# Optimization experiments

Measured on AMD Instinct MI355X. Metric: run time of the kernel, lower is better.

## Reference

```python
import jax, jax.numpy as jnp
import numpy as np
import math

D = 768
H = 12
HD = D // H  # 64
B, N = 16, 1024
EPS = 1e-5


def _rope(x, cos, sin):
    # x: [B,N,H,hd]; cos,sin: [1,N,1,hd]
    x1, x2 = x[..., ::2], x[..., 1::2]
    return jnp.concatenate(
        [x1 * cos[..., ::2] - x2 * sin[..., ::2],
         x1 * sin[..., 1::2] + x2 * cos[..., 1::2]], axis=-1)


def setup_inputs() -> dict:
    key = jax.random.key(0)
    ks = jax.random.split(key, 8)
    s = 1.0 / math.sqrt(D)  # xavier-ish scale
    return {
        "x": jax.random.normal(ks[0], (B, N, D), jnp.float32),
        "rope_emb": jax.random.normal(ks[1], (N, HD), jnp.float32),
        "ln_w": jnp.ones((D,), jnp.float32),
        "ln_b": jnp.zeros((D,), jnp.float32),
        "enc_w": jax.random.normal(ks[2], (D, D), jnp.float32) * s,
        "enc_b": jnp.zeros((D,), jnp.float32),
        "qk_w": jax.random.normal(ks[3], (D, D), jnp.float32) * s,
        "qk_b": jnp.zeros((D,), jnp.float32),
        "v_w": jax.random.normal(ks[4], (D, D), jnp.float32) * s,
        "v_b": jnp.zeros((D,), jnp.float32),
        "out_w": jax.random.normal(ks[5], (D, D), jnp.float32) * s,
        "out_b": jnp.zeros((D,), jnp.float32),
        "gate_w": jax.random.normal(ks[6], (D, D), jnp.float32) * s,
        "gate_b": jnp.zeros((D,), jnp.float32),
    }


def reference(x, rope_emb, ln_w, ln_b, enc_w, enc_b, qk_w, qk_b,
              v_w, v_b, out_w, out_b, gate_w, gate_b):
    b, n, d = x.shape
    # Pre-LayerNorm
    mu = jnp.mean(x, axis=-1, keepdims=True)
    var = jnp.mean(jnp.square(x - mu), axis=-1, keepdims=True)
    x_norm = (x - mu) / jnp.sqrt(var + EPS) * ln_w + ln_b
    # sparse latent encoder
    x_latent = jax.nn.relu(x_norm @ enc_w.T + enc_b)
    qk = (x_latent @ qk_w.T + qk_b).reshape(b, n, H, HD)
    v = (x_latent @ v_w.T + v_b).reshape(b, n, H, HD)
    ang = rope_emb[:, :HD]
    cos = jnp.cos(ang)[None, :, None, :]
    sin = jnp.sin(ang)[None, :, None, :]
    qk = _rope(qk, cos, sin)
    # raw (softmax-free) attention, Q=K
    scores = jnp.einsum('bnhd,bmhd->bhnm', qk, qk) / math.sqrt(HD)
    attn = jnp.einsum('bhnm,bmhd->bnhd', scores, v).reshape(b, n, d)
    attn = attn @ out_w.T + out_b
    gate = jax.nn.sigmoid(x_norm @ gate_w.T + gate_b)
    return x + gate * attn
```

## Files before the change

### kernel.cpp

```cpp
#include <hip/hip_runtime.h>

typedef __bf16 bf16;
typedef __bf16 bf16x2 __attribute__((ext_vector_type(2)));
typedef __bf16 bf16x4 __attribute__((ext_vector_type(4)));
typedef __bf16 bf16x8 __attribute__((ext_vector_type(8)));
typedef float floatx4 __attribute__((ext_vector_type(4)));

#define DD 768
#define NH 12
#define HDIM 64
#define BB 16
#define NN 1024
#define MTOT (BB*NN)
#define WELEM (DD*DD)

#define ABUF 16384
#define BBUF 8192
#define TBUF (ABUF + BBUF)

__device__ __forceinline__ void async_cp16(const void* g, void* l) {
  __builtin_amdgcn_global_load_lds((const __attribute__((address_space(1))) void*)g,
                                   (__attribute__((address_space(3))) void*)l, 16, 0, 0);
}

__global__ __launch_bounds__(256) void prep_kernel(
    const float* __restrict__ x, const float* __restrict__ lnw,
    const float* __restrict__ lnb, bf16* __restrict__ A,
    const float* __restrict__ w0, const float* __restrict__ w1,
    const float* __restrict__ w2, const float* __restrict__ w3,
    const float* __restrict__ w4, bf16* __restrict__ Wb,
    const float* __restrict__ rope, float* __restrict__ tabs) {
  int blk = blockIdx.x;
  int tid = threadIdx.x;
  if (blk < 4096) {
    int row = blk * 4 + (tid >> 6);
    int lane = tid & 63;
    const float4* xr = (const float4*)(x + (size_t)row * DD);
    float4 v[3];
    float s = 0.f;
#pragma unroll
    for (int i = 0; i < 3; i++) {
      v[i] = xr[lane + 64 * i];
      s += v[i].x + v[i].y + v[i].z + v[i].w;
    }
#pragma unroll
    for (int o = 32; o; o >>= 1) s += __shfl_xor(s, o);
    float mu = s * (1.f / 768.f);
    float vs = 0.f;
#pragma unroll
    for (int i = 0; i < 3; i++) {
      float dx;
      dx = v[i].x - mu; vs += dx * dx;
      dx = v[i].y - mu; vs += dx * dx;
      dx = v[i].z - mu; vs += dx * dx;
      dx = v[i].w - mu; vs += dx * dx;
    }
#pragma unroll
    for (int o = 32; o; o >>= 1) vs += __shfl_xor(vs, o);
    float rstd = rsqrtf(vs * (1.f / 768.f) + 1e-5f);
    const float4* wv = (const float4*)lnw;
    const float4* bv = (const float4*)lnb;
    bf16* Ar = A + (size_t)row * DD;
#pragma unroll
    for (int i = 0; i < 3; i++) {
      int c4 = lane + 64 * i;
      float4 ww = wv[c4], bb = bv[c4];
      bf16x4 pk;
      pk[0] = (bf16)((v[i].x - mu) * rstd * ww.x + bb.x);
      pk[1] = (bf16)((v[i].y - mu) * rstd * ww.y + bb.y);
      pk[2] = (bf16)((v[i].z - mu) * rstd * ww.z + bb.z);
      pk[3] = (bf16)((v[i].w - mu) * rstd * ww.w + bb.w);
      *(bf16x4*)(Ar + c4 * 4) = pk;
    }
  } else if (blk < 4096 + 2880) {
    int i = (blk - 4096) * 256 + tid;
    int which = i / (WELEM / 4);
    int off = (i % (WELEM / 4)) * 4;
    const float* s = which == 0 ? w0 : which == 1 ? w1 : which == 2 ? w2 : which == 3 ? w3 : w4;
    float4 v = *(const float4*)(s + off);
    bf16x4 pk;
    pk[0] = (bf16)v.x; pk[1] = (bf16)v.y; pk[2] = (bf16)v.z; pk[3] = (bf16)v.w;
    *(bf16x4*)(Wb + (size_t)i * 4) = pk;
  } else {
    int i = (blk - 6976) * 256 + tid;
    int j = i >> 10, n = i & 1023;
    float a = rope[n * 64 + j];
    float s, c;
    __sincosf(a, &s, &c);
    tabs[i] = c;
    tabs[65536 + i] = s;
  }
}

template<int EPI>
__device__ __forceinline__ void gemm_body(
    int bm, int bn, int bnl,
    const bf16* __restrict__ Aop, const bf16* __restrict__ W,
    const float* __restrict__ bias,
    bf16* __restrict__ Cb, bf16* __restrict__ CT, float* __restrict__ Cf,
    const float* __restrict__ Xres, const bf16* __restrict__ Gate,
    const float* __restrict__ tabs, bf16* smem) {
  int tid = threadIdx.x;
  int w = tid >> 6, lane = tid & 63;
  int quad = lane >> 4, l16 = lane & 15;
  int wm = w >> 1, wn = w & 1;
  int sr = lane >> 3;
  int scg = (lane & 7) ^ sr;
  int swz = l16 & 7;

  const bf16* Ag = Aop + (size_t)(bm * 256) * DD;
  const bf16* Bg = W + (size_t)(bn * 128) * DD;
  const bf16* srcA = Ag + (size_t)(w * 8 + sr) * DD + scg * 8;
  const bf16* srcB = Bg + (size_t)(w * 8 + sr) * DD + scg * 8;

  floatx4 acc[4][4];
#pragma unroll
  for (int i = 0; i < 4; i++)
#pragma unroll
    for (int j = 0; j < 4; j++)
      acc[i][j] = (floatx4){0.f, 0.f, 0.f, 0.f};

  auto stageH0 = [&](int k0, bf16* buf) {
    async_cp16(srcA + (size_t)0 * (64 * DD) + k0, buf + (w + 0) * 512);
    async_cp16(srcA + (size_t)1 * (64 * DD) + k0, buf + (w + 8) * 512);
    async_cp16(srcB + k0, buf + ABUF + w * 512);
  };
  auto stageH1 = [&](int k0, bf16* buf) {
    async_cp16(srcA + (size_t)2 * (64 * DD) + k0, buf + (w + 16) * 512);
    async_cp16(srcA + (size_t)3 * (64 * DD) + k0, buf + (w + 24) * 512);
    async_cp16(srcB + (size_t)64 * DD + k0, buf + ABUF + (w + 8) * 512);
  };

  stageH0(0, smem);               stageH1(0, smem);
  stageH0(64, smem + TBUF);       stageH1(64, smem + TBUF);

#pragma unroll
  for (int t = 0; t < 12; t++) {
    if (t < 11) asm volatile("s_waitcnt vmcnt(6)" ::: "memory");
    else        asm volatile("s_waitcnt vmcnt(0)" ::: "memory");
    __builtin_amdgcn_s_barrier();
    __builtin_amdgcn_sched_barrier(0);

    const bf16* Ab = smem + (t % 3) * TBUF;
    const bf16* Bb = Ab + ABUF;
#pragma unroll
    for (int ks = 0; ks < 2; ks++) {
      int cg = (ks * 4 + quad) ^ swz;
      bf16x8 a[4], b[4];
#pragma unroll
      for (int i = 0; i < 4; i++) a[i] = *(const bf16x8*)&Ab[(wm * 64 + i * 16 + l16) * 64 + cg * 8];
#pragma unroll
      for (int i = 0; i < 4; i++) b[i] = *(const bf16x8*)&Bb[(wn * 64 + i * 16 + l16) * 64 + cg * 8];
      if (t < 10) {
        if (ks == 0) stageH0((t + 2) * 64, smem + ((t + 2) % 3) * TBUF);
        else         stageH1((t + 2) * 64, smem + ((t + 2) % 3) * TBUF);
      }
      __builtin_amdgcn_s_barrier();
      __builtin_amdgcn_sched_barrier(0);
      asm volatile("s_waitcnt lgkmcnt(0)" ::: "memory");
      __builtin_amdgcn_sched_barrier(0);
      __builtin_amdgcn_s_setprio(1);
      if (EPI == 2) {
#pragma unroll
        for (int mi = 0; mi < 4; mi++)
#pragma unroll
          for (int ni = 0; ni < 4; ni++)
            acc[mi][ni] = __builtin_amdgcn_mfma_f32_16x16x32_bf16(a[mi], b[ni], acc[mi][ni], 0, 0, 0);
      } else {
#pragma unroll
        for (int mi = 0; mi < 4; mi++)
#pragma unroll
          for (int ni = 0; ni < 4; ni++)
            acc[mi][ni] = __builtin_amdgcn_mfma_f32_16x16x32_bf16(b[ni], a[mi], acc[mi][ni], 0, 0, 0);
      }
      __builtin_amdgcn_s_setprio(0);
    }
  }

  if (EPI == 2) {
#pragma unroll
    for (int ni = 0; ni < 4; ni++) {
      int gc = bnl * 128 + wn * 64 + ni * 16 + l16;
      float bz = bias[gc];
      int h = gc >> 6, dd2 = gc & 63;
#pragma unroll
      for (int mi = 0; mi < 4; mi++) {
        int gm0 = bm * 256 + wm * 64 + mi * 16 + quad * 4;
        int b_ = gm0 >> 10, n0 = gm0 & 1023;
        bf16x4 pk;
#pragma unroll
        for (int r = 0; r < 4; r++) pk[r] = (bf16)(acc[mi][ni][r] + bz);
        *(bf16x4*)&Cb[(((size_t)b_ * NH + h) * HDIM + dd2) * NN + n0] = pk;
      }
    }
  } else if (EPI == 5) {
    const int ST2H = 256 * 72;
    bf16* st2 = smem;
    const float* cTb = tabs;
    const float* sTb = tabs + 65536;
    __syncthreads();
#pragma unroll
    for (int mi = 0; mi < 4; mi++) {
      int gm = bm * 256 + wm * 64 + mi * 16 + l16;
      int n = gm & 1023, n_local = gm & 255;
#pragma unroll
      for (int ni = 0; ni < 4; ni++) {
        int gc = bnl * 128 + wn * 64 + ni * 16 + quad * 4;
        float4 bz = *(const float4*)&bias[gc];
        float v0 = acc[mi][ni][0] + bz.x;
        float v1 = acc[mi][ni][1] + bz.y;
        float v2 = acc[mi][ni][2] + bz.z;
        float v3 = acc[mi][ni][3] + bz.w;
        int j2 = gc & 63;
        float c0 = cTb[(j2 + 0) * 1024 + n];
        float c1 = cTb[(j2 + 1) * 1024 + n];
        float c2 = cTb[(j2 + 2) * 1024 + n];
        float c3 = cTb[(j2 + 3) * 1024 + n];
        float s0 = sTb[(j2 + 0) * 1024 + n];
        float s1 = sTb[(j2 + 1) * 1024 + n];
        float s2 = sTb[(j2 + 2) * 1024 + n];
        float s3 = sTb[(j2 + 3) * 1024 + n];
        bf16x2 e0, e1;
        e0[0] = (bf16)(v0 * c0 - v1 * s0);
        e0[1] = (bf16)(v2 * c2 - v3 * s2);
        e1[0] = (bf16)(v0 * s1 + v1 * c1);
        e1[1] = (bf16)(v2 * s3 + v3 * c3);
        int p0 = j2 >> 1;
        bf16* rowp = st2 + wn * ST2H + n_local * 72;
        *(bf16x2*)&rowp[p0] = e0;
        *(bf16x2*)&rowp[32 + p0] = e1;
      }
    }
    __syncthreads();
    {
      int n_local = tid >> 1, hh = tid & 1;
      int gm = bm * 256 + n_local;
      int h = bnl * 2 + hh;
      bf16* dst = Cb + (size_t)gm * DD + h * 64;
      const bf16* srcr = st2 + hh * ST2H + n_local * 72;
#pragma unroll
      for (int j = 0; j < 8; j++)
        *(bf16x8*)&dst[j * 8] = *(const bf16x8*)&srcr[j * 8];
    }
    {
      int row = tid >> 2, part = tid & 3;
      int hh = row >> 6, p = row & 63;
      int b_ = bm >> 2;
      int h = bnl * 2 + hh;
      __attribute__((aligned(16))) bf16 buf[64];
#pragma unroll
      for (int k = 0; k < 64; k++)
        buf[k] = st2[hh * ST2H + (part * 64 + k) * 72 + p];
      bf16* dst = CT + ((size_t)(b_ * NH + h) * HDIM + p) * NN + (bm & 3) * 256 + part * 64;
#pragma unroll
      for (int j = 0; j < 8; j++)
        *(bf16x8*)&dst[j * 8] = *(const bf16x8*)&buf[j * 8];
    }
  } else if (EPI == 4) {
#pragma unroll
    for (int mi = 0; mi < 4; mi++) {
      int gm = bm * 256 + wm * 64 + mi * 16 + l16;
#pragma unroll
      for (int ni = 0; ni < 4; ni++) {
        int gc = bnl * 128 + wn * 64 + ni * 16 + quad * 4;
        float4 bz = *(const float4*)&bias[gc];
        float v0 = acc[mi][ni][0] + bz.x;
        float v1 = acc[mi][ni][1] + bz.y;
        float v2 = acc[mi][ni][2] + bz.z;
        float v3 = acc[mi][ni][3] + bz.w;
        size_t idx = (size_t)gm * DD + gc;
        bf16x4 g = *(const bf16x4*)&Gate[idx];
        float4 xr = *(const float4*)&Xres[idx];
        float4 o;
        o.x = xr.x + (float)g[0] * v0;
        o.y = xr.y + (float)g[1] * v1;
        o.z = xr.z + (float)g[2] * v2;
        o.w = xr.w + (float)g[3] * v3;
        *(float4*)&Cf[idx] = o;
      }
    }
  } else {
    const int SPC = 136;
    bf16* st = smem;
    __syncthreads();
#pragma unroll
    for (int mi = 0; mi < 4; mi++) {
      int rloc = wm * 64 + mi * 16 + l16;
#pragma unroll
      for (int ni = 0; ni < 4; ni++) {
        int cloc = wn * 64 + ni * 16 + quad * 4;
        int gc = bnl * 128 + cloc;
        float4 bz = *(const float4*)&bias[gc];
        float v0 = acc[mi][ni][0] + bz.x;
        float v1 = acc[mi][ni][1] + bz.y;
        float v2 = acc[mi][ni][2] + bz.z;
        float v3 = acc[mi][ni][3] + bz.w;
        bf16x4 pk;
        if (EPI == 0) {
          pk[0] = (bf16)fmaxf(v0, 0.f); pk[1] = (bf16)fmaxf(v1, 0.f);
          pk[2] = (bf16)fmaxf(v2, 0.f); pk[3] = (bf16)fmaxf(v3, 0.f);
        } else if (EPI == 1) {
          pk[0] = (bf16)v0; pk[1] = (bf16)v1; pk[2] = (bf16)v2; pk[3] = (bf16)v3;
        } else {
          pk[0] = (bf16)(1.f / (1.f + __expf(-v0)));
          pk[1] = (bf16)(1.f / (1.f + __expf(-v1)));
          pk[2] = (bf16)(1.f / (1.f + __expf(-v2)));
          pk[3] = (bf16)(1.f / (1.f + __expf(-v3)));
        }
        *(bf16x4*)&st[rloc * SPC + cloc] = pk;
      }
    }
    __syncthreads();
    {
      int row = tid >> 1, half = tid & 1;
      int gm = bm * 256 + row;
      bf16* dst = Cb + (size_t)gm * DD + bnl * 128 + half * 64;
      const bf16* sr = &st[row * SPC + half * 64];
#pragma unroll
      for (int j = 0; j < 8; j++)
        *(bf16x8*)&dst[j * 8] = *(const bf16x8*)&sr[j * 8];
    }
  }
}

template<int EPI_LO, int EPI_HI, int NBN>
__global__ __launch_bounds__(512, 2) void gemm_kernel(
    const bf16* __restrict__ Aop, const bf16* __restrict__ W,
    const float* __restrict__ bias_lo, const float* __restrict__ bias_hi,
    bf16* __restrict__ C_lo, bf16* __restrict__ C_hi, bf16* __restrict__ CT,
    float* __restrict__ Cf,
    const float* __restrict__ Xres, const bf16* __restrict__ Gate,
    const float* __restrict__ tabs) {
  __shared__ __attribute__((aligned(16))) bf16 smem[3 * TBUF];
  int blk = blockIdx.x;
  int xcd = blk & 7, slot = blk >> 3;
  int bm = xcd * 8 + slot / NBN;
  int bn = slot % NBN;
  if (NBN == 12 && bn >= 6) {
    gemm_body<EPI_HI>(bm, bn, bn - 6, Aop, W, bias_hi, C_hi, CT, Cf, Xres, Gate, tabs, smem);
  } else {
    gemm_body<EPI_LO>(bm, bn, bn, Aop, W, bias_lo, C_lo, CT, Cf, Xres, Gate, tabs, smem);
  }
}

template<int EPI>
__device__ __forceinline__ void gemm0_body(
    int bm, int bn, int bnl,
    const bf16* __restrict__ Aop, const bf16* __restrict__ W,
    const float* __restrict__ bias,
    bf16* __restrict__ Cb, float* __restrict__ Cf,
    const float* __restrict__ Xres, const bf16* __restrict__ Gate,
    bf16* As, bf16* Bs) {
  int tid = threadIdx.x;
  int wave = tid >> 6, lane = tid & 63;
  int quad = lane >> 4, l16 = lane & 15;
  int wm = wave & 1, wn = wave >> 1;
  int sr = lane >> 3;
  int smcg = (lane & 7) ^ sr;

  const bf16* Ag = Aop + (size_t)(bm * 256) * DD;
  const bf16* Bg = W + (size_t)(bn * 128) * DD;

  floatx4 acc[8][4];
#pragma unroll
  for (int i = 0; i < 8; i++)
#pragma unroll
    for (int j = 0; j < 4; j++)
      acc[i][j] = (floatx4){0.f, 0.f, 0.f, 0.f};

  int swzA = (l16 & 7);

  for (int k0 = 0; k0 < DD; k0 += 64) {
    __syncthreads();
#pragma unroll
    for (int it = 0; it < 8; it++) {
      int c = it * 4 + wave;
      int row = c * 8 + sr;
      async_cp16(Ag + (size_t)row * DD + k0 + smcg * 8, &As[c * 512]);
    }
#pragma unroll
    for (int it = 0; it < 4; it++) {
      int c = it * 4 + wave;
      int row = c * 8 + sr;
      async_cp16(Bg + (size_t)row * DD + k0 + smcg * 8, &Bs[c * 512]);
    }
    __syncthreads();
#pragma unroll
    for (int ks = 0; ks < 2; ks++) {
      int cg = (ks * 4 + quad) ^ swzA;
      bf16x8 a[8], b[4];
#pragma unroll
      for (int i = 0; i < 8; i++) a[i] = *(const bf16x8*)&As[(wm * 128 + i * 16 + l16) * 64 + cg * 8];
#pragma unroll
      for (int i = 0; i < 4; i++) b[i] = *(const bf16x8*)&Bs[(wn * 64 + i * 16 + l16) * 64 + cg * 8];
#pragma unroll
      for (int mi = 0; mi < 8; mi++)
#pragma unroll
        for (int ni = 0; ni < 4; ni++)
          acc[mi][ni] = __builtin_amdgcn_mfma_f32_16x16x32_bf16(b[ni], a[mi], acc[mi][ni], 0, 0, 0);
    }
  }

#pragma unroll
  for (int mi = 0; mi < 8; mi++) {
    int gm = bm * 256 + wm * 128 + mi * 16 + l16;
#pragma unroll
    for (int ni = 0; ni < 4; ni++) {
      int gc = bnl * 128 + wn * 64 + ni * 16 + quad * 4;
      float4 bz = *(const float4*)&bias[gc];
      float v0 = acc[mi][ni][0] + bz.x;
      float v1 = acc[mi][ni][1] + bz.y;
      float v2 = acc[mi][ni][2] + bz.z;
      float v3 = acc[mi][ni][3] + bz.w;
      size_t idx = (size_t)gm * DD + gc;
      if (EPI == 4) {
        bf16x4 g = *(const bf16x4*)&Gate[idx];
        float4 xr = *(const float4*)&Xres[idx];
        float4 o;
        o.x = xr.x + (float)g[0] * v0;
        o.y = xr.y + (float)g[1] * v1;
        o.z = xr.z + (float)g[2] * v2;
        o.w = xr.w + (float)g[3] * v3;
        *(float4*)&Cf[idx] = o;
      } else {
        bf16x4 pk;
        pk[0] = (bf16)v0; pk[1] = (bf16)v1; pk[2] = (bf16)v2; pk[3] = (bf16)v3;
        *(bf16x4*)&Cb[idx] = pk;
      }
    }
  }
}

template<int EPI, int NBN>
__global__ __launch_bounds__(256, 2) void gemm0_kernel(
    const bf16* __restrict__ Aop, const bf16* __restrict__ W,
    const float* __restrict__ bias,
    bf16* __restrict__ Cb, float* __restrict__ Cf,
    const float* __restrict__ Xres, const bf16* __restrict__ Gate) {
  __shared__ bf16 As[256 * 64];
  __shared__ bf16 Bs[128 * 64];
  int blk = blockIdx.x;
  int xcd = blk & 7, slot = blk >> 3;
  int bm = xcd * 8 + slot / NBN;
  int bn = slot % NBN;
  gemm0_body<EPI>(bm, bn, bn, Aop, W, bias, Cb, Cf, Xres, Gate, As, Bs);
}

__global__ __launch_bounds__(256) void attn_kernel(const bf16* __restrict__ QKr,
    const bf16* __restrict__ QKrT, const bf16* __restrict__ VT, bf16* __restrict__ attn) {
  __shared__ float Tp[64][64];
  __shared__ bf16 Tbf[64][72];
  int blk = blockIdx.x;
  int xcd = blk & 7, bhl = blk >> 3;
  int bh = xcd * 24 + bhl;
  int tid = threadIdx.x, wave = tid >> 6, lane = tid & 63;
  int quad = lane >> 4, l16 = lane & 15;
  const bf16* Qt = QKrT + (size_t)bh * (HDIM * NN);
  const bf16* Vt = VT + (size_t)bh * (HDIM * NN);

  floatx4 acc[4][4];
#pragma unroll
  for (int i = 0; i < 4; i++)
#pragma unroll
    for (int j = 0; j < 4; j++)
      acc[i][j] = (floatx4){0.f, 0.f, 0.f, 0.f};

  int kbase = wave * 256;
#pragma unroll
  for (int k0 = 0; k0 < 256; k0 += 32) {
    bf16x8 a[4], b[4];
#pragma unroll
    for (int i = 0; i < 4; i++) a[i] = *(const bf16x8*)&Qt[(size_t)(i * 16 + l16) * NN + kbase + k0 + quad * 8];
#pragma unroll
    for (int i = 0; i < 4; i++) b[i] = *(const bf16x8*)&Vt[(size_t)(i * 16 + l16) * NN + kbase + k0 + quad * 8];
#pragma unroll
    for (int mi = 0; mi < 4; mi++)
#pragma unroll
      for (int ni = 0; ni < 4; ni++)
        acc[mi][ni] = __builtin_amdgcn_mfma_f32_16x16x32_bf16(a[mi], b[ni], acc[mi][ni], 0, 0, 0);
  }
#pragma unroll
  for (int w = 0; w < 4; w++) {
    if (wave == w) {
#pragma unroll
      for (int mi = 0; mi < 4; mi++)
#pragma unroll
        for (int ni = 0; ni < 4; ni++)
#pragma unroll
          for (int r = 0; r < 4; r++) {
            float val = acc[mi][ni][r];
            float* p = &Tp[mi * 16 + quad * 4 + r][ni * 16 + l16];
            if (w == 0) *p = val; else *p += val;
          }
    }
    __syncthreads();
  }
  for (int e = tid; e < 4096; e += 256) {
    int d1 = e >> 6, d2 = e & 63;
    Tbf[d2][d1] = (bf16)(Tp[d1][d2] * 0.125f);
  }
  __syncthreads();

  int b_ = bh / NH, h_ = bh % NH;
  const bf16* Q = QKr + (size_t)(b_ * NN) * DD + h_ * HDIM;
  bf16* Ao = attn + (size_t)(b_ * NN) * DD + h_ * HDIM;
  bf16x8 Bf[4][2];
#pragma unroll
  for (int ni = 0; ni < 4; ni++)
#pragma unroll
    for (int ks = 0; ks < 2; ks++)
      Bf[ni][ks] = *(const bf16x8*)&Tbf[ni * 16 + l16][ks * 32 + quad * 8];

#pragma unroll
  for (int mi = 0; mi < 16; mi++) {
    int nrow = wave * 256 + mi * 16;
    bf16x8 a0 = *(const bf16x8*)&Q[(size_t)(nrow + l16) * DD + quad * 8];
    bf16x8 a1 = *(const bf16x8*)&Q[(size_t)(nrow + l16) * DD + 32 + quad * 8];
    floatx4 o[4];
#pragma unroll
    for (int ni = 0; ni < 4; ni++) o[ni] = (floatx4){0.f, 0.f, 0.f, 0.f};
#pragma unroll
    for (int ni = 0; ni < 4; ni++) {
      o[ni] = __builtin_amdgcn_mfma_f32_16x16x32_bf16(Bf[ni][0], a0, o[ni], 0, 0, 0);
      o[ni] = __builtin_amdgcn_mfma_f32_16x16x32_bf16(Bf[ni][1], a1, o[ni], 0, 0, 0);
    }
#pragma unroll
    for (int ni = 0; ni < 4; ni++) {
      bf16x4 pk;
#pragma unroll
      for (int r = 0; r < 4; r++) pk[r] = (bf16)o[ni][r];
      *(bf16x4*)&Ao[(size_t)(nrow + l16) * DD + ni * 16 + quad * 4] = pk;
    }
  }
}

extern "C" void kernel_launch(void* const* d_in, const int* in_sizes, int n_in,
                              void* d_out, int out_size, void* d_ws, size_t ws_size,
                              hipStream_t stream) {
  const float* x      = (const float*)d_in[0];
  const float* rope   = (const float*)d_in[1];
  const float* ln_w   = (const float*)d_in[2];
  const float* ln_b   = (const float*)d_in[3];
  const float* enc_w  = (const float*)d_in[4];
  const float* enc_b  = (const float*)d_in[5];
  const float* qk_w   = (const float*)d_in[6];
  const float* qk_b   = (const float*)d_in[7];
  const float* v_w    = (const float*)d_in[8];
  const float* v_b    = (const float*)d_in[9];
  const float* out_w  = (const float*)d_in[10];
  const float* out_b  = (const float*)d_in[11];
  const float* gate_w = (const float*)d_in[12];
  const float* gate_b = (const float*)d_in[13];

  char* w = (char*)d_ws;
  const size_t S = (size_t)MTOT * DD * 2;
  bf16* s0 = (bf16*)(w);
  bf16* s1 = (bf16*)(w + S);
  bf16* s2 = (bf16*)(w + 2 * S);
  bf16* s3 = (bf16*)(w + 3 * S);
  bf16* s4 = (bf16*)(w + 4 * S);
  bf16* s5 = (bf16*)(w + 5 * S);
  bf16* Wb = (bf16*)(w + 6 * S);
  float* tabs = (float*)(w + 6 * S + 6 * 1024 * 1024);

  bf16* A = s0;
  bf16* L = s1;
  bf16* Gate = s2;
  bf16* QKr = s3;
  bf16* QKrT = s4;
  bf16* VT = s5;
  bf16* attnb = s1;

  prep_kernel<<<dim3(7232), dim3(256), 0, stream>>>(
      x, ln_w, ln_b, A, enc_w, gate_w, qk_w, v_w, out_w, Wb, rope, tabs);

  gemm_kernel<0, 3, 12><<<dim3(768), dim3(512), 0, stream>>>(
      A, Wb, enc_b, gate_b, L, Gate, nullptr, nullptr, nullptr, nullptr, nullptr);
  gemm_kernel<5, 2, 12><<<dim3(768), dim3(512), 0, stream>>>(
      L, Wb + 2 * (size_t)WELEM, qk_b, v_b, QKr, VT, QKrT, nullptr, nullptr, nullptr, tabs);
  attn_kernel<<<dim3(BB * NH), dim3(256), 0, stream>>>(QKr, QKrT, VT, attnb);
  gemm0_kernel<4, 6><<<dim3(384), dim3(256), 0, stream>>>(
      attnb, Wb + 4 * (size_t)WELEM, out_b, nullptr, (float*)d_out, x, Gate);
}
```

Measured before the change: 321.7 us.

## Enlarge fused GEMM tiles to 256x256 with double-buffered staggered loads

```diff
diff --git a/kernel.cpp b/kernel.cpp
--- a/kernel.cpp
+++ b/kernel.cpp
@@ -13,10 +13,6 @@
 #define NN 1024
 #define MTOT (BB*NN)
 #define WELEM (DD*DD)
-
-#define ABUF 16384
-#define BBUF 8192
-#define TBUF (ABUF + BBUF)
 
 __device__ __forceinline__ void async_cp16(const void* g, void* l) {
   __builtin_amdgcn_global_load_lds((const __attribute__((address_space(1))) void*)g,
@@ -93,99 +89,146 @@
 }
 
 template<int EPI>
-__device__ __forceinline__ void gemm_body(
+__device__ __forceinline__ void gemm8_body(
     int bm, int bn, int bnl,
     const bf16* __restrict__ Aop, const bf16* __restrict__ W,
     const float* __restrict__ bias,
-    bf16* __restrict__ Cb, bf16* __restrict__ CT, float* __restrict__ Cf,
-    const float* __restrict__ Xres, const bf16* __restrict__ Gate,
+    bf16* __restrict__ Cb, bf16* __restrict__ CT,
     const float* __restrict__ tabs, bf16* smem) {
   int tid = threadIdx.x;
   int w = tid >> 6, lane = tid & 63;
   int quad = lane >> 4, l16 = lane & 15;
-  int wm = w >> 1, wn = w & 1;
+  int wm = w >> 2, wn = w & 3;
   int sr = lane >> 3;
   int scg = (lane & 7) ^ sr;
   int swz = l16 & 7;
 
   const bf16* Ag = Aop + (size_t)(bm * 256) * DD;
-  const bf16* Bg = W + (size_t)(bn * 128) * DD;
-  const bf16* srcA = Ag + (size_t)(w * 8 + sr) * DD + scg * 8;
-  const bf16* srcB = Bg + (size_t)(w * 8 + sr) * DD + scg * 8;
-
-  floatx4 acc[4][4];
-#pragma unroll
-  for (int i = 0; i < 4; i++)
+  const bf16* Bg = W + (size_t)(bn * 256) * DD;
+
+  floatx4 acc[8][4];
+#pragma unroll
+  for (int i = 0; i < 8; i++)
 #pragma unroll
     for (int j = 0; j < 4; j++)
       acc[i][j] = (floatx4){0.f, 0.f, 0.f, 0.f};
 
-  auto stageH0 = [&](int k0, bf16* buf) {
-    async_cp16(srcA + (size_t)0 * (64 * DD) + k0, buf + (w + 0) * 512);
-    async_cp16(srcA + (size_t)1 * (64 * DD) + k0, buf + (w + 8) * 512);
-    async_cp16(srcB + k0, buf + ABUF + w * 512);
+  auto stage_unit = [&](int unit, int t) {
+    const bf16* base = (unit < 2) ? (Ag + (size_t)(unit * 128) * DD)
+                                  : (Bg + (size_t)((unit - 2) * 128) * DD);
+    const bf16* s0 = base + (size_t)(w * 8 + sr) * DD + t * 64 + scg * 8;
+    bf16* d = smem + (t & 1) * 32768 + unit * 8192 + w * 512;
+    async_cp16(s0, d);
+    async_cp16(s0 + (size_t)64 * DD, d + 4096);
   };
-  auto stageH1 = [&](int k0, bf16* buf) {
-    async_cp16(srcA + (size_t)2 * (64 * DD) + k0, buf + (w + 16) * 512);
-    async_cp16(srcA + (size_t)3 * (64 * DD) + k0, buf + (w + 24) * 512);
-    async_cp16(srcB + (size_t)64 * DD + k0, buf + ABUF + (w + 8) * 512);
+
+  stage_unit(0, 0); stage_unit(1, 0); stage_unit(2, 0); stage_unit(3, 0);
+  stage_unit(0, 1); stage_unit(1, 1);
+  asm volatile("s_waitcnt vmcnt(4)" ::: "memory");
+  __builtin_amdgcn_s_barrier();
+  __builtin_amdgcn_sched_barrier(0);
+
+  bf16x8 af[2][4], bq[2][2];
+
+  auto MF = [&](int mib, int nib) {
+    __builtin_amdgcn_s_setprio(1);
+#pragma unroll
+    for (int ks = 0; ks < 2; ks++)
+#pragma unroll
+      for (int i = 0; i < 4; i++)
+#pragma unroll
+        for (int j = 0; j < 2; j++) {
+          if (EPI == 2)
+            acc[mib + i][nib + j] = __builtin_amdgcn_mfma_f32_16x16x32_bf16(
+                af[ks][i], bq[ks][j], acc[mib + i][nib + j], 0, 0, 0);
+          else
+            acc[mib + i][nib + j] = __builtin_amdgcn_mfma_f32_16x16x32_bf16(
+                bq[ks][j], af[ks][i], acc[mib + i][nib + j], 0, 0, 0);
+        }
+    __builtin_amdgcn_s_setprio(0);
   };
 
-  stageH0(0, smem);               stageH1(0, smem);
-  stageH0(64, smem + TBUF);       stageH1(64, smem + TBUF);
-
 #pragma unroll
   for (int t = 0; t < 12; t++) {
-    if (t < 11) asm volatile("s_waitcnt vmcnt(6)" ::: "memory");
-    else        asm volatile("s_waitcnt vmcnt(0)" ::: "memory");
-    __builtin_amdgcn_s_barrier();
-    __builtin_amdgcn_sched_barrier(0);
-
-    const bf16* Ab = smem + (t % 3) * TBUF;
-    const bf16* Bb = Ab + ABUF;
+    const bf16* buf = smem + (t & 1) * 32768;
+    const bf16* Au = buf + wm * 8192;
+    const bf16* Bu = buf + (2 + (wn >> 1)) * 8192;
+    int br = (wn & 1) * 64;
+
 #pragma unroll
     for (int ks = 0; ks < 2; ks++) {
       int cg = (ks * 4 + quad) ^ swz;
-      bf16x8 a[4], b[4];
-#pragma unroll
-      for (int i = 0; i < 4; i++) a[i] = *(const bf16x8*)&Ab[(wm * 64 + i * 16 + l16) * 64 + cg * 8];
-#pragma unroll
-      for (int i = 0; i < 4; i++) b[i] = *(const bf16x8*)&Bb[(wn * 64 + i * 16 + l16) * 64 + cg * 8];
-      if (t < 10) {
-        if (ks == 0) stageH0((t + 2) * 64, smem + ((t + 2) % 3) * TBUF);
-        else         stageH1((t + 2) * 64, smem + ((t + 2) % 3) * TBUF);
-      }
-      __builtin_amdgcn_s_barrier();
-      __builtin_amdgcn_sched_barrier(0);
-      asm volatile("s_waitcnt lgkmcnt(0)" ::: "memory");
-      __builtin_amdgcn_sched_barrier(0);
-      __builtin_amdgcn_s_setprio(1);
-      if (EPI == 2) {
-#pragma unroll
-        for (int mi = 0; mi < 4; mi++)
-#pragma unroll
-          for (int ni = 0; ni < 4; ni++)
-            acc[mi][ni] = __builtin_amdgcn_mfma_f32_16x16x32_bf16(a[mi], b[ni], acc[mi][ni], 0, 0, 0);
-      } else {
-#pragma unroll
-        for (int mi = 0; mi < 4; mi++)
-#pragma unroll
-          for (int ni = 0; ni < 4; ni++)
-            acc[mi][ni] = __builtin_amdgcn_mfma_f32_16x16x32_bf16(b[ni], a[mi], acc[mi][ni], 0, 0, 0);
-      }
-      __builtin_amdgcn_s_setprio(0);
-    }
+#pragma unroll
+      for (int i = 0; i < 4; i++)
+        af[ks][i] = *(const bf16x8*)&Au[(i * 16 + l16) * 64 + cg * 8];
+#pragma unroll
+      for (int j = 0; j < 2; j++)
+        bq[ks][j] = *(const bf16x8*)&Bu[(br + j * 16 + l16) * 64 + cg * 8];
+    }
+    if (t <= 10) stage_unit(2, t + 1);
+    __builtin_amdgcn_s_barrier();
+    asm volatile("s_waitcnt lgkmcnt(0)" ::: "memory");
+    __builtin_amdgcn_sched_barrier(0);
+    MF(0, 0);
+    __builtin_amdgcn_s_barrier();
+    __builtin_amdgcn_sched_barrier(0);
+
+#pragma unroll
+    for (int ks = 0; ks < 2; ks++) {
+      int cg = (ks * 4 + quad) ^ swz;
+#pragma unroll
+      for (int j = 0; j < 2; j++)
+        bq[ks][j] = *(const bf16x8*)&Bu[(br + 32 + j * 16 + l16) * 64 + cg * 8];
+    }
+    if (t <= 10) stage_unit(3, t + 1);
+    __builtin_amdgcn_s_barrier();
+    asm volatile("s_waitcnt lgkmcnt(0)" ::: "memory");
+    __builtin_amdgcn_sched_barrier(0);
+    MF(0, 2);
+    __builtin_amdgcn_s_barrier();
+    __builtin_amdgcn_sched_barrier(0);
+
+#pragma unroll
+    for (int ks = 0; ks < 2; ks++) {
+      int cg = (ks * 4 + quad) ^ swz;
+#pragma unroll
+      for (int i = 0; i < 4; i++)
+        af[ks][i] = *(const bf16x8*)&Au[(64 + i * 16 + l16) * 64 + cg * 8];
+    }
+    __builtin_amdgcn_s_barrier();
+    asm volatile("s_waitcnt lgkmcnt(0)" ::: "memory");
+    __builtin_amdgcn_sched_barrier(0);
+    MF(4, 2);
+    __builtin_amdgcn_s_barrier();
+    __builtin_amdgcn_sched_barrier(0);
+
+#pragma unroll
+    for (int ks = 0; ks < 2; ks++) {
+      int cg = (ks * 4 + quad) ^ swz;
+#pragma unroll
+      for (int j = 0; j < 2; j++)
+        bq[ks][j] = *(const bf16x8*)&Bu[(br + j * 16 + l16) * 64 + cg * 8];
+    }
+    if (t <= 9) { stage_unit(0, t + 2); stage_unit(1, t + 2); }
+    __builtin_amdgcn_s_barrier();
+    asm volatile("s_waitcnt lgkmcnt(0)" ::: "memory");
+    __builtin_amdgcn_sched_barrier(0);
+    MF(4, 0);
+    if (t < 10)       asm volatile("s_waitcnt vmcnt(4)" ::: "memory");
+    else if (t == 10) asm volatile("s_waitcnt vmcnt(0)" ::: "memory");
+    __builtin_amdgcn_s_barrier();
+    __builtin_amdgcn_sched_barrier(0);
   }
 
   if (EPI == 2) {
 #pragma unroll
     for (int ni = 0; ni < 4; ni++) {
-      int gc = bnl * 128 + wn * 64 + ni * 16 + l16;
+      int gc = bnl * 256 + wn * 64 + ni * 16 + l16;
       float bz = bias[gc];
       int h = gc >> 6, dd2 = gc & 63;
 #pragma unroll
-      for (int mi = 0; mi < 4; mi++) {
-        int gm0 = bm * 256 + wm * 64 + mi * 16 + quad * 4;
+      for (int mi = 0; mi < 8; mi++) {
+        int gm0 = bm * 256 + wm * 128 + mi * 16 + quad * 4;
         int b_ = gm0 >> 10, n0 = gm0 & 1023;
         bf16x4 pk;
 #pragma unroll
@@ -198,148 +241,133 @@
     bf16* st2 = smem;
     const float* cTb = tabs;
     const float* sTb = tabs + 65536;
-    __syncthreads();
-#pragma unroll
-    for (int mi = 0; mi < 4; mi++) {
-      int gm = bm * 256 + wm * 64 + mi * 16 + l16;
-      int n = gm & 1023, n_local = gm & 255;
-#pragma unroll
-      for (int ni = 0; ni < 4; ni++) {
-        int gc = bnl * 128 + wn * 64 + ni * 16 + quad * 4;
-        float4 bz = *(const float4*)&bias[gc];
-        float v0 = acc[mi][ni][0] + bz.x;
-        float v1 = acc[mi][ni][1] + bz.y;
-        float v2 = acc[mi][ni][2] + bz.z;
-        float v3 = acc[mi][ni][3] + bz.w;
-        int j2 = gc & 63;
-        float c0 = cTb[(j2 + 0) * 1024 + n];
-        float c1 = cTb[(j2 + 1) * 1024 + n];
-        float c2 = cTb[(j2 + 2) * 1024 + n];
-        float c3 = cTb[(j2 + 3) * 1024 + n];
-        float s0 = sTb[(j2 + 0) * 1024 + n];
-        float s1 = sTb[(j2 + 1) * 1024 + n];
-        float s2 = sTb[(j2 + 2) * 1024 + n];
-        float s3 = sTb[(j2 + 3) * 1024 + n];
-        bf16x2 e0, e1;
-        e0[0] = (bf16)(v0 * c0 - v1 * s0);
-        e0[1] = (bf16)(v2 * c2 - v3 * s2);
-        e1[0] = (bf16)(v0 * s1 + v1 * c1);
-        e1[1] = (bf16)(v2 * s3 + v3 * c3);
-        int p0 = j2 >> 1;
-        bf16* rowp = st2 + wn * ST2H + n_local * 72;
-        *(bf16x2*)&rowp[p0] = e0;
-        *(bf16x2*)&rowp[32 + p0] = e1;
+#pragma unroll
+    for (int P = 0; P < 2; P++) {
+      __syncthreads();
+      if ((wn >> 1) == P) {
+#pragma unroll
+        for (int mi = 0; mi < 8; mi++) {
+          int gm = bm * 256 + wm * 128 + mi * 16 + l16;
+          int n = gm & 1023, n_local = gm & 255;
+#pragma unroll
+          for (int ni = 0; ni < 4; ni++) {
+            int j2 = ni * 16 + quad * 4;
+            int gc = bnl * 256 + wn * 64 + j2;
+            float4 bz = *(const float4*)&bias[gc];
+            float v0 = acc[mi][ni][0] + bz.x;
+            float v1 = acc[mi][ni][1] + bz.y;
+            float v2 = acc[mi][ni][2] + bz.z;
+            float v3 = acc[mi][ni][3] + bz.w;
+            float c0 = cTb[(j2 + 0) * 1024 + n];
+            float c1 = cTb[(j2 + 1) * 1024 + n];
+            float c2 = cTb[(j2 + 2) * 1024 + n];
+            float c3 = cTb[(j2 + 3) * 1024 + n];
+            float s0 = sTb[(j2 + 0) * 1024 + n];
+            float s1 = sTb[(j2 + 1) * 1024 + n];
+            float s2 = sTb[(j2 + 2) * 1024 + n];
+            float s3 = sTb[(j2 + 3) * 1024 + n];
+            bf16x2 e0, e1;
+            e0[0] = (bf16)(v0 * c0 - v1 * s0);
+            e0[1] = (bf16)(v2 * c2 - v3 * s2);
+            e1[0] = (bf16)(v0 * s1 + v1 * c1);
+            e1[1] = (bf16)(v2 * s3 + v3 * c3);
+            int p0 = j2 >> 1;
+            bf16* rowp = st2 + (wn & 1) * ST2H + n_local * 72;
+            *(bf16x2*)&rowp[p0] = e0;
+            *(bf16x2*)&rowp[32 + p0] = e1;
+          }
+        }
       }
-    }
-    __syncthreads();
-    {
-      int n_local = tid >> 1, hh = tid & 1;
-      int gm = bm * 256 + n_local;
-      int h = bnl * 2 + hh;
-      bf16* dst = Cb + (size_t)gm * DD + h * 64;
-      const bf16* srcr = st2 + hh * ST2H + n_local * 72;
-#pragma unroll
-      for (int j = 0; j < 8; j++)
-        *(bf16x8*)&dst[j * 8] = *(const bf16x8*)&srcr[j * 8];
-    }
-    {
-      int row = tid >> 2, part = tid & 3;
-      int hh = row >> 6, p = row & 63;
-      int b_ = bm >> 2;
-      int h = bnl * 2 + hh;
-      __attribute__((aligned(16))) bf16 buf[64];
-#pragma unroll
-      for (int k = 0; k < 64; k++)
-        buf[k] = st2[hh * ST2H + (part * 64 + k) * 72 + p];
-      bf16* dst = CT + ((size_t)(b_ * NH + h) * HDIM + p) * NN + (bm & 3) * 256 + part * 64;
-#pragma unroll
-      for (int j = 0; j < 8; j++)
-        *(bf16x8*)&dst[j * 8] = *(const bf16x8*)&buf[j * 8];
-    }
-  } else if (EPI == 4) {
-#pragma unroll
-    for (int mi = 0; mi < 4; mi++) {
-      int gm = bm * 256 + wm * 64 + mi * 16 + l16;
-#pragma unroll
-      for (int ni = 0; ni < 4; ni++) {
-        int gc = bnl * 128 + wn * 64 + ni * 16 + quad * 4;
-        float4 bz = *(const float4*)&bias[gc];
-        float v0 = acc[mi][ni][0] + bz.x;
-        float v1 = acc[mi][ni][1] + bz.y;
-        float v2 = acc[mi][ni][2] + bz.z;
-        float v3 = acc[mi][ni][3] + bz.w;
-        size_t idx = (size_t)gm * DD + gc;
-        bf16x4 g = *(const bf16x4*)&Gate[idx];
-        float4 xr = *(const float4*)&Xres[idx];
-        float4 o;
-        o.x = xr.x + (float)g[0] * v0;
-        o.y = xr.y + (float)g[1] * v1;
-        o.z = xr.z + (float)g[2] * v2;
-        o.w = xr.w + (float)g[3] * v3;
-        *(float4*)&Cf[idx] = o;
+      __syncthreads();
+      {
+        int n_local = tid >> 1, hh = tid & 1;
+        int gm = bm * 256 + n_local;
+        int h = bnl * 4 + P * 2 + hh;
+        bf16* dst = Cb + (size_t)gm * DD + h * 64;
+        const bf16* srcr = st2 + hh * ST2H + n_local * 72;
+#pragma unroll
+        for (int j = 0; j < 8; j++)
+          *(bf16x8*)&dst[j * 8] = *(const bf16x8*)&srcr[j * 8];
+      }
+      {
+        int row = tid >> 2, part = tid & 3;
+        int hh = row >> 6, p = row & 63;
+        int b_ = bm >> 2;
+        int h = bnl * 4 + P * 2 + hh;
+        __attribute__((aligned(16))) bf16 buf[64];
+#pragma unroll
+        for (int k = 0; k < 64; k++)
+          buf[k] = st2[hh * ST2H + (part * 64 + k) * 72 + p];
+        bf16* dst = CT + ((size_t)(b_ * NH + h) * HDIM + p) * NN + (bm & 3) * 256 + part * 64;
+#pragma unroll
+        for (int j = 0; j < 8; j++)
+          *(bf16x8*)&dst[j * 8] = *(const bf16x8*)&buf[j * 8];
       }
     }
   } else {
     const int SPC = 136;
     bf16* st = smem;
-    __syncthreads();
-#pragma unroll
-    for (int mi = 0; mi < 4; mi++) {
-      int rloc = wm * 64 + mi * 16 + l16;
-#pragma unroll
-      for (int ni = 0; ni < 4; ni++) {
-        int cloc = wn * 64 + ni * 16 + quad * 4;
-        int gc = bnl * 128 + cloc;
-        float4 bz = *(const float4*)&bias[gc];
-        float v0 = acc[mi][ni][0] + bz.x;
-        float v1 = acc[mi][ni][1] + bz.y;
-        float v2 = acc[mi][ni][2] + bz.z;
-        float v3 = acc[mi][ni][3] + bz.w;
-        bf16x4 pk;
-        if (EPI == 0) {
-          pk[0] = (bf16)fmaxf(v0, 0.f); pk[1] = (bf16)fmaxf(v1, 0.f);
-          pk[2] = (bf16)fmaxf(v2, 0.f); pk[3] = (bf16)fmaxf(v3, 0.f);
-        } else if (EPI == 1) {
-          pk[0] = (bf16)v0; pk[1] = (bf16)v1; pk[2] = (bf16)v2; pk[3] = (bf16)v3;
-        } else {
-          pk[0] = (bf16)(1.f / (1.f + __expf(-v0)));
-          pk[1] = (bf16)(1.f / (1.f + __expf(-v1)));
-          pk[2] = (bf16)(1.f / (1.f + __expf(-v2)));
-          pk[3] = (bf16)(1.f / (1.f + __expf(-v3)));
+#pragma unroll
+    for (int P = 0; P < 2; P++) {
+      __syncthreads();
+      if ((wn >> 1) == P) {
+#pragma unroll
+        for (int mi = 0; mi < 8; mi++) {
+          int rloc = wm * 128 + mi * 16 + l16;
+#pragma unroll
+          for (int ni = 0; ni < 4; ni++) {
+            int cl = (wn & 1) * 64 + ni * 16 + quad * 4;
+            int gc = bnl * 256 + P * 128 + cl;
+            float4 bz = *(const float4*)&bias[gc];
+            float v0 = acc[mi][ni][0] + bz.x;
+            float v1 = acc[mi][ni][1] + bz.y;
+            float v2 = acc[mi][ni][2] + bz.z;
+            float v3 = acc[mi][ni][3] + bz.w;
+            bf16x4 pk;
+            if (EPI == 0) {
+              pk[0] = (bf16)fmaxf(v0, 0.f); pk[1] = (bf16)fmaxf(v1, 0.f);
+              pk[2] = (bf16)fmaxf(v2, 0.f); pk[3] = (bf16)fmaxf(v3, 0.f);
+            } else if (EPI == 1) {
+              pk[0] = (bf16)v0; pk[1] = (bf16)v1; pk[2] = (bf16)v2; pk[3] = (bf16)v3;
+            } else {
+              pk[0] = (bf16)(1.f / (1.f + __expf(-v0)));
+              pk[1] = (bf16)(1.f / (1.f + __expf(-v1)));
+              pk[2] = (bf16)(1.f / (1.f + __expf(-v2)));
+              pk[3] = (bf16)(1.f / (1.f + __expf(-v3)));
+            }
+            *(bf16x4*)&st[rloc * SPC + cl] = pk;
+          }
         }
-        *(bf16x4*)&st[rloc * SPC + cloc] = pk;
       }
-    }
-    __syncthreads();
-    {
-      int row = tid >> 1, half = tid & 1;
-      int gm = bm * 256 + row;
-      bf16* dst = Cb + (size_t)gm * DD + bnl * 128 + half * 64;
-      const bf16* sr = &st[row * SPC + half * 64];
-#pragma unroll
-      for (int j = 0; j < 8; j++)
-        *(bf16x8*)&dst[j * 8] = *(const bf16x8*)&sr[j * 8];
-    }
-  }
-}
-
-template<int EPI_LO, int EPI_HI, int NBN>
-__global__ __launch_bounds__(512, 2) void gemm_kernel(
+      __syncthreads();
+      {
+        int row = tid >> 1, half = tid & 1;
+        int gm = bm * 256 + row;
+        bf16* dst = Cb + (size_t)gm * DD + bnl * 256 + P * 128 + half * 64;
+        const bf16* sr2 = &st[row * SPC + half * 64];
+#pragma unroll
+        for (int j = 0; j < 8; j++)
+          *(bf16x8*)&dst[j * 8] = *(const bf16x8*)&sr2[j * 8];
+      }
+    }
+  }
+}
+
+template<int EPI_LO, int EPI_HI>
+__global__ __launch_bounds__(512, 2) void gemm8_kernel(
     const bf16* __restrict__ Aop, const bf16* __restrict__ W,
     const float* __restrict__ bias_lo, const float* __restrict__ bias_hi,
     bf16* __restrict__ C_lo, bf16* __restrict__ C_hi, bf16* __restrict__ CT,
-    float* __restrict__ Cf,
-    const float* __restrict__ Xres, const bf16* __restrict__ Gate,
     const float* __restrict__ tabs) {
-  __shared__ __attribute__((aligned(16))) bf16 smem[3 * TBUF];
+  __shared__ __attribute__((aligned(16))) bf16 smem[65536];
   int blk = blockIdx.x;
   int xcd = blk & 7, slot = blk >> 3;
-  int bm = xcd * 8 + slot / NBN;
-  int bn = slot % NBN;
-  if (NBN == 12 && bn >= 6) {
-    gemm_body<EPI_HI>(bm, bn, bn - 6, Aop, W, bias_hi, C_hi, CT, Cf, Xres, Gate, tabs, smem);
+  int bm = xcd * 8 + slot / 6;
+  int bn = slot % 6;
+  if (bn >= 3) {
+    gemm8_body<EPI_HI>(bm, bn, bn - 3, Aop, W, bias_hi, C_hi, CT, tabs, smem);
   } else {
-    gemm_body<EPI_LO>(bm, bn, bn, Aop, W, bias_lo, C_lo, CT, Cf, Xres, Gate, tabs, smem);
+    gemm8_body<EPI_LO>(bm, bn, bn, Aop, W, bias_lo, C_lo, CT, tabs, smem);
   }
 }
 
@@ -574,10 +602,10 @@
   prep_kernel<<<dim3(7232), dim3(256), 0, stream>>>(
       x, ln_w, ln_b, A, enc_w, gate_w, qk_w, v_w, out_w, Wb, rope, tabs);
 
-  gemm_kernel<0, 3, 12><<<dim3(768), dim3(512), 0, stream>>>(
-      A, Wb, enc_b, gate_b, L, Gate, nullptr, nullptr, nullptr, nullptr, nullptr);
-  gemm_kernel<5, 2, 12><<<dim3(768), dim3(512), 0, stream>>>(
-      L, Wb + 2 * (size_t)WELEM, qk_b, v_b, QKr, VT, QKrT, nullptr, nullptr, nullptr, tabs);
+  gemm8_kernel<0, 3><<<dim3(384), dim3(512), 0, stream>>>(
+      A, Wb, enc_b, gate_b, L, Gate, nullptr, tabs);
+  gemm8_kernel<5, 2><<<dim3(384), dim3(512), 0, stream>>>(
+      L, Wb + 2 * (size_t)WELEM, qk_b, v_b, QKr, VT, QKrT, tabs);
   attn_kernel<<<dim3(BB * NH), dim3(256), 0, stream>>>(QKr, QKrT, VT, attnb);
   gemm0_kernel<4, 6><<<dim3(384), dim3(256), 0, stream>>>(
       attnb, Wb + 4 * (size_t)WELEM, out_b, nullptr, (float*)d_out, x, Gate);
```

Result: slower. 367.2 us (+14.2%).
